# Performance work log

Hardware: AMD Instinct MI355X
Metric: run time of the kernel (lower is better)

Reference implementation:

```python
import jax, jax.numpy as jnp
import numpy as np

DIM = 96
D_STATE = 16
EXPAND = 2
D_INNER = EXPAND * DIM
DT_RANK = (DIM + 15) // 16  # 6
B, H, W = 2, 64, 64
K = 4  # scan directions


def _ln(x, w, b, eps=1e-5):
    mu = x.mean(-1, keepdims=True)
    var = x.var(-1, keepdims=True)
    return (x - mu) / jnp.sqrt(var + eps) * w + b


def setup_inputs() -> dict:
    key = jax.random.key(0)
    ks = jax.random.split(key, 10)
    f = jnp.float32
    x = jax.random.normal(ks[0], (B, H, W, DIM), dtype=f)
    y = jax.random.normal(ks[1], (B, H, W, DIM), dtype=f)
    inp = {
        'x': x,
        'y': y,
        'ln_w': jnp.ones((DIM,), f),
        'ln_b': jnp.zeros((DIM,), f),
        'in_proj_w': jax.random.normal(ks[2], (2 * D_INNER, DIM), f) * 0.05,
        'conv_w': jax.random.normal(ks[3], (D_INNER, 1, 3, 3), f) * 0.1,
        'conv_b': jnp.zeros((D_INNER,), f),
        'x_proj_w': jax.random.normal(ks[4], (K, DT_RANK + 2 * D_STATE, D_INNER), f) * 0.05,
        'dt_w': jax.random.normal(ks[5], (K, D_INNER, DT_RANK), f) * 0.1,
        'dt_b': jax.random.normal(ks[6], (K, D_INNER), f) * 0.1,
        'A_log': jnp.broadcast_to(jnp.log(jnp.arange(1, D_STATE + 1, dtype=f)), (K, D_INNER, D_STATE)),
        'Ds': jnp.ones((K, D_INNER), f),
        'out_norm_w': jnp.ones((D_INNER,), f),
        'out_norm_b': jnp.zeros((D_INNER,), f),
        'out_proj_w': jax.random.normal(ks[7], (DIM, D_INNER), f) * 0.05,
    }
    return inp


def _fwd(x, y, ln_w, ln_b, in_proj_w, conv_w, conv_b, x_proj_w, dt_w, dt_b,
         A_log, Ds, out_norm_w, out_norm_b, out_proj_w):
    Bsz, Hh, Ww, C = x.shape
    Din = conv_w.shape[0]
    N = A_log.shape[-1]
    R = dt_w.shape[-1]
    L = Hh * Ww

    diff = jnp.abs(x - y)                       # TemporalSpectrumBlock abs-diff
    h = _ln(diff, ln_w, ln_b)                   # VSSBlock ln_1
    xz = h @ in_proj_w.T                        # (B,H,W,2*Din)
    xm, z = jnp.split(xz, 2, axis=-1)
    xm = xm.transpose(0, 3, 1, 2)               # (B,Din,H,W)
    xm = jax.lax.conv_general_dilated(
        xm, conv_w, (1, 1), 'SAME', feature_group_count=Din,
        dimension_numbers=('NCHW', 'OIHW', 'NCHW')) + conv_b[None, :, None, None]
    xm = jax.nn.silu(xm)

    # 4-directional sequences (B,4,Din,L)
    x0 = xm.reshape(Bsz, Din, L)
    x1 = xm.transpose(0, 1, 3, 2).reshape(Bsz, Din, L)
    xs = jnp.stack([x0, x1], axis=1)
    xs = jnp.concatenate([xs, jnp.flip(xs, axis=-1)], axis=1)

    x_dbl = jnp.einsum('bkdl,kcd->bkcl', xs, x_proj_w)
    dts, Bs, Cs = jnp.split(x_dbl, [R, R + N], axis=2)   # (B,4,R,L),(B,4,N,L),(B,4,N,L)
    dts = jnp.einsum('bkrl,kdr->bkdl', dts, dt_w)
    delta = jax.nn.softplus(dts + dt_b[None, :, :, None])  # (B,4,Din,L)

    A = -jnp.exp(A_log)                                    # (4,Din,N)
    dA = jnp.exp(delta[..., None] * A[None, :, :, None, :])          # (B,4,Din,L,N)
    dBu = delta[..., None] * Bs.transpose(0, 1, 3, 2)[:, :, None] * xs[..., None]

    dA_t = dA.transpose(3, 0, 1, 2, 4)    # (L,B,4,Din,N)
    dBu_t = dBu.transpose(3, 0, 1, 2, 4)
    C_t = Cs.transpose(3, 0, 1, 2)        # (L,B,4,N)
    h0 = jnp.zeros((Bsz, 4, Din, N), dtype=x.dtype)

    def step(hc, inp):
        a, bu, c = inp
        hc = a * hc + bu
        yv = jnp.einsum('bkdn,bkn->bkd', hc, c)
        return hc, yv

    _, ys = jax.lax.scan(step, h0, (dA_t, dBu_t, C_t))    # (L,B,4,Din)
    ys = ys.transpose(1, 2, 3, 0)                          # (B,4,Din,L)
    out_y = ys + Ds[None, :, :, None] * xs

    inv_y = jnp.flip(out_y[:, 2:4], axis=-1)
    wh_y = out_y[:, 1].reshape(Bsz, Din, Ww, Hh).transpose(0, 1, 3, 2).reshape(Bsz, Din, L)
    invwh_y = inv_y[:, 1].reshape(Bsz, Din, Ww, Hh).transpose(0, 1, 3, 2).reshape(Bsz, Din, L)
    yc = out_y[:, 0] + inv_y[:, 0] + wh_y + invwh_y        # (B,Din,L)
    yc = yc.transpose(0, 2, 1).reshape(Bsz, Hh, Ww, Din)

    yn = _ln(yc, out_norm_w, out_norm_b)
    out = (yn * jax.nn.silu(z)) @ out_proj_w.T
    return diff + out                                      # residual around the block


def reference(x, y, ln_w, ln_b, in_proj_w, conv_w, conv_b, x_proj_w, dt_w, dt_b,
              A_log, Ds, out_norm_w, out_norm_b, out_proj_w):
    return _fwd(x, y, ln_w, ln_b, in_proj_w, conv_w, conv_b, x_proj_w, dt_w, dt_b,
                A_log, Ds, out_norm_w, out_norm_b, out_proj_w)
```

## Files before the change

kernel.cpp:

```cpp
#include <hip/hip_runtime.h>
#include <math.h>

#define DIMC 96
#define DIN  192
#define NST  16
#define RNK  6
#define KD   4
#define HH   64
#define WWD  64
#define LL   4096
#define BB   2
#define NC   64
#define CH   64
#define CPK  48

__device__ __forceinline__ int pos_of(int k, int l) {
    int t = ((l & 63) << 6) | (l >> 6);
    switch (k) {
        case 0: return l;
        case 1: return t;
        case 2: return LL - 1 - l;
        default: return ((((LL-1-l) & 63) << 6) | ((LL-1-l) >> 6));
    }
}

__device__ __forceinline__ float silu_f(float v) {
    return v / (1.f + __expf(-v));
}

__global__ __launch_bounds__(256) void k0_prep(
    const float* __restrict__ Win, const float* __restrict__ Wout,
    const float* __restrict__ xpw,
    float* __restrict__ WinT, float* __restrict__ WoutT, float* __restrict__ wT3)
{
    int idx = blockIdx.x*256 + threadIdx.x;
    int stride = gridDim.x*256;
    for (int i = idx; i < 96*384; i += stride) {
        int j = i / 384, o = i - j*384;
        WinT[i] = Win[o*96 + j];
    }
    for (int i = idx; i < 192*96; i += stride) {
        int j = i / 96, o = i - j*96;
        WoutT[i] = Wout[o*192 + j];
    }
    for (int i = idx; i < KD*192*CPK; i += stride) {
        int kk = i / (192*CPK); int rem = i - kk*192*CPK;
        int j = rem / CPK, c = rem - j*CPK;
        float v = 0.f;
        if (c < 16)       v = xpw[((size_t)kk*(RNK+2*NST) + RNK + c)*DIN + j];
        else if (c < 32)  v = xpw[((size_t)kk*(RNK+2*NST) + RNK + NST + (c-16))*DIN + j];
        else if (c < 38)  v = xpw[((size_t)kk*(RNK+2*NST) + (c-32))*DIN + j];
        wT3[i] = v;
    }
}

__global__ __launch_bounds__(1024) void k1_ln_inproj(
    const float* __restrict__ x, const float* __restrict__ y,
    const float* __restrict__ lnw, const float* __restrict__ lnb,
    const float* __restrict__ WinT,
    float* __restrict__ diff, float* __restrict__ xm, float* __restrict__ zbuf)
{
    __shared__ float hT[96*65];
    __shared__ float ps1[16*64], ps2[16*64];
    __shared__ float mus[64], rss[64];
    int t = threadIdx.x;
    int ptile = blockIdx.x >> 1, cgrp = blockIdx.x & 1;
    int p0 = ptile*64;

    #pragma unroll
    for (int s = 0; s < 6; s++) {
        int i = t + 1024*s;
        float v = fabsf(x[(size_t)p0*96 + i] - y[(size_t)p0*96 + i]);
        if (cgrp == 0) diff[(size_t)p0*96 + i] = v;
        int pos = i / 96, ch = i - pos*96;
        hT[ch*65 + pos] = v;
    }
    __syncthreads();
    {
        int pos = t & 63, part = t >> 6;
        float s1 = 0.f, s2 = 0.f;
        #pragma unroll
        for (int m = 0; m < 6; m++) {
            float v = hT[(part*6 + m)*65 + pos];
            s1 += v; s2 += v*v;
        }
        ps1[part*64 + pos] = s1; ps2[part*64 + pos] = s2;
    }
    __syncthreads();
    if (t < 64) {
        float S1 = 0.f, S2 = 0.f;
        #pragma unroll
        for (int i = 0; i < 16; i++) { S1 += ps1[i*64 + t]; S2 += ps2[i*64 + t]; }
        float mu = S1 * (1.f/96.f);
        float var = S2 * (1.f/96.f) - mu*mu;
        mus[t] = mu; rss[t] = rsqrtf(var + 1e-5f);
    }
    __syncthreads();
    #pragma unroll
    for (int s = 0; s < 6; s++) {
        int i = t + 1024*s;
        int pos = i / 96, ch = i - pos*96;
        hT[ch*65 + pos] = (hT[ch*65 + pos] - mus[pos]) * rss[pos] * lnw[ch] + lnb[ch];
    }
    __syncthreads();

    int w = __builtin_amdgcn_readfirstlane(t >> 6);
    int lane = t & 63;
    int c0 = cgrp*192 + w*12;
    const float* wp = WinT + c0;
    float acc[12];
    #pragma unroll
    for (int cc = 0; cc < 12; cc++) acc[cc] = 0.f;
    #pragma unroll 2
    for (int j = 0; j < 96; j++) {
        float u = hT[j*65 + lane];
        const float* wrow = wp + j*384;
        #pragma unroll
        for (int cc = 0; cc < 12; cc++) acc[cc] += u * wrow[cc];
    }
    size_t p = (size_t)(p0 + lane);
    float* dst = (c0 < 192) ? (xm + p*192 + c0) : (zbuf + p*192 + (c0 - 192));
    #pragma unroll
    for (int q = 0; q < 3; q++)
        *(float4*)&dst[4*q] = make_float4(acc[4*q], acc[4*q+1], acc[4*q+2], acc[4*q+3]);
}

__global__ __launch_bounds__(192) void k2_conv(
    const float* __restrict__ xm, const float* __restrict__ cw,
    const float* __restrict__ cb, float* __restrict__ xconv)
{
    int p = blockIdx.x;
    int d = threadIdx.x;
    int b = p >> 12;
    int l = p & (LL - 1);
    int hh = l >> 6, ww = l & 63;
    float acc = cb[d];
    const float* wd = cw + d*9;
    #pragma unroll
    for (int di = -1; di <= 1; di++) {
        int h2 = hh + di;
        if ((unsigned)h2 < HH) {
            #pragma unroll
            for (int dj = -1; dj <= 1; dj++) {
                int w2 = ww + dj;
                if ((unsigned)w2 < WWD)
                    acc += wd[(di+1)*3 + (dj+1)] * xm[((size_t)b*LL + h2*WWD + w2)*DIN + d];
            }
        }
    }
    xconv[(size_t)p*DIN + d] = silu_f(acc);
}

__global__ __launch_bounds__(512) void k3_xproj(
    const float* __restrict__ xconv, const float* __restrict__ wT3,
    float* __restrict__ XDK)
{
    __shared__ float uT[192*65];
    int t = threadIdx.x;
    int ptile = blockIdx.x >> 1, wgrp = blockIdx.x & 1;
    int p0 = ptile*64;

    #pragma unroll
    for (int s = 0; s < 24; s++) {
        int i = t + 512*s;
        int pos = i / 192, ch = i - pos*192;
        uT[ch*65 + pos] = xconv[(size_t)(p0 + pos)*192 + ch];
    }
    __syncthreads();

    int w = __builtin_amdgcn_readfirstlane(t >> 6);
    int slot = wgrp*8 + w;
    int k = slot >> 2, cq = slot & 3;
    int lane = t & 63;
    int c0 = cq*12;
    const float* wp = wT3 + (size_t)k*192*CPK + c0;
    float acc[12];
    #pragma unroll
    for (int cc = 0; cc < 12; cc++) acc[cc] = 0.f;
    #pragma unroll 2
    for (int j = 0; j < 192; j++) {
        float u = uT[j*65 + lane];
        const float* wrow = wp + j*CPK;
        #pragma unroll
        for (int cc = 0; cc < 12; cc++) acc[cc] += u * wrow[cc];
    }
    int p = p0 + lane;
    int b = p >> 12;
    int s = p & (LL - 1);
    int ts = ((s & 63) << 6) | (s >> 6);
    int l;
    switch (k) {
        case 0: l = s; break;
        case 1: l = ts; break;
        case 2: l = LL - 1 - s; break;
        default: l = LL - 1 - ts; break;
    }
    float* dst = XDK + ((size_t)(b*KD + k)*LL + l)*CPK + c0;
    #pragma unroll
    for (int q = 0; q < 3; q++)
        *(float4*)&dst[4*q] = make_float4(acc[4*q], acc[4*q+1], acc[4*q+2], acc[4*q+3]);
}

__global__ __launch_bounds__(192) void k4_scanA(
    const float* __restrict__ xconv, const float* __restrict__ XDK,
    const float* __restrict__ dtw, const float* __restrict__ dtb,
    const float* __restrict__ A_log,
    float* __restrict__ P, float* __restrict__ Q)
{
    int blk = blockIdx.x;
    int c  = blk & (NC - 1);
    int bk = blk >> 6;
    int k  = bk & 3;
    int b  = bk >> 2;
    int d  = threadIdx.x;
    float dw[RNK];
    #pragma unroll
    for (int r = 0; r < RNK; r++) dw[r] = dtw[((size_t)k*DIN + d)*RNK + r];
    float bias = dtb[k*DIN + d];
    float A[NST];
    #pragma unroll
    for (int n = 0; n < NST; n++) A[n] = -__expf(A_log[((size_t)k*DIN + d)*NST + n]);

    float h[NST], pr[NST];
    #pragma unroll
    for (int n = 0; n < NST; n++) { h[n] = 0.f; pr[n] = 1.f; }

    size_t rb = ((size_t)bk*LL + c*CH)*CPK;
    #pragma unroll 2
    for (int step = 0; step < CH; step++) {
        const float* rec = XDK + rb + step*CPK;
        float dl = bias;
        #pragma unroll
        for (int r = 0; r < RNK; r++) dl += rec[32 + r] * dw[r];
        dl = (dl > 20.f) ? dl : __logf(1.f + __expf(dl));
        int l = c*CH + step;
        float uu = xconv[((size_t)b*LL + pos_of(k, l))*DIN + d];
        float du = dl * uu;
        #pragma unroll
        for (int n = 0; n < NST; n++) {
            float a = __expf(dl * A[n]);
            h[n] = a*h[n] + du*rec[n];
            pr[n] *= a;
        }
    }
    size_t base = (size_t)blk*NST*DIN + d;
    #pragma unroll
    for (int n = 0; n < NST; n++) { P[base + n*DIN] = pr[n]; Q[base + n*DIN] = h[n]; }
}

__global__ __launch_bounds__(256) void k5_scanB(
    const float* __restrict__ P, float* __restrict__ Q)
{
    int idx = blockIdx.x*256 + threadIdx.x;
    if (idx >= BB*KD*NST*DIN) return;
    int d = idx % DIN;
    int rest = idx / DIN;
    int n = rest % NST; rest /= NST;
    int k = rest % KD;
    int b = rest / KD;
    size_t base = ((((size_t)(b*KD + k))*NC)*NST + n)*DIN + d;
    size_t stride = (size_t)NST*DIN;
    float h = 0.f;
    #pragma unroll 4
    for (int c = 0; c < NC; c++) {
        float p = P[base + c*stride];
        float q = Q[base + c*stride];
        Q[base + c*stride] = h;
        h = p*h + q;
    }
}

__global__ __launch_bounds__(192) void k6_scanC(
    const float* __restrict__ xconv, const float* __restrict__ XDK,
    const float* __restrict__ dtw, const float* __restrict__ dtb,
    const float* __restrict__ A_log, const float* __restrict__ Ds,
    const float* __restrict__ Q, float* __restrict__ outy)
{
    int blk = blockIdx.x;
    int c  = blk & (NC - 1);
    int bk = blk >> 6;
    int k  = bk & 3;
    int b  = bk >> 2;
    int d  = threadIdx.x;
    float dw[RNK];
    #pragma unroll
    for (int r = 0; r < RNK; r++) dw[r] = dtw[((size_t)k*DIN + d)*RNK + r];
    float bias = dtb[k*DIN + d];
    float A[NST];
    #pragma unroll
    for (int n = 0; n < NST; n++) A[n] = -__expf(A_log[((size_t)k*DIN + d)*NST + n]);
    float h[NST];
    size_t qbase = (size_t)blk*NST*DIN + d;
    #pragma unroll
    for (int n = 0; n < NST; n++) h[n] = Q[qbase + n*DIN];
    float Dv = Ds[k*DIN + d];

    size_t rb = ((size_t)bk*LL + c*CH)*CPK;
    #pragma unroll 2
    for (int step = 0; step < CH; step++) {
        const float* rec = XDK + rb + step*CPK;
        float dl = bias;
        #pragma unroll
        for (int r = 0; r < RNK; r++) dl += rec[32 + r] * dw[r];
        dl = (dl > 20.f) ? dl : __logf(1.f + __expf(dl));
        int l = c*CH + step;
        float uu = xconv[((size_t)b*LL + pos_of(k, l))*DIN + d];
        float du = dl * uu;
        float yv = 0.f;
        #pragma unroll
        for (int n = 0; n < NST; n++) {
            float a = __expf(dl * A[n]);
            h[n] = a*h[n] + du*rec[n];
            yv += h[n] * rec[16 + n];
        }
        outy[((size_t)bk*LL + l)*DIN + d] = yv + Dv*uu;
    }
}

__global__ __launch_bounds__(256) void k7_out(
    const float* __restrict__ outy, const float* __restrict__ zbuf,
    const float* __restrict__ diff, const float* __restrict__ onw,
    const float* __restrict__ onb, const float* __restrict__ WoutT,
    float* __restrict__ out)
{
    __shared__ float gT[192*65];
    __shared__ float ps1[4*64], ps2[4*64];
    __shared__ float mus[64], rss[64];
    int t = threadIdx.x;
    int ptile = blockIdx.x >> 1, chalf = blockIdx.x & 1;
    int p0 = ptile*64;
    int b = p0 >> 12;
    int l0 = p0 & (LL - 1);

    #pragma unroll
    for (int s = 0; s < 48; s++) {
        int i = t + 256*s;
        int pos = i / 192, ch = i - pos*192;
        int l = l0 + pos;
        int tl = ((l & 63) << 6) | (l >> 6);
        float yc = outy[(((size_t)(b*KD + 0))*LL + l)*DIN + ch]
                 + outy[(((size_t)(b*KD + 2))*LL + (LL-1-l))*DIN + ch]
                 + outy[(((size_t)(b*KD + 1))*LL + tl)*DIN + ch]
                 + outy[(((size_t)(b*KD + 3))*LL + (LL-1-tl))*DIN + ch];
        gT[ch*65 + pos] = yc;
    }
    __syncthreads();
    {
        int pos = t & 63, part = t >> 6;
        float s1 = 0.f, s2 = 0.f;
        #pragma unroll
        for (int m = 0; m < 48; m++) {
            float v = gT[(part*48 + m)*65 + pos];
            s1 += v; s2 += v*v;
        }
        ps1[part*64 + pos] = s1; ps2[part*64 + pos] = s2;
    }
    __syncthreads();
    if (t < 64) {
        float S1 = ps1[t] + ps1[64+t] + ps1[128+t] + ps1[192+t];
        float S2 = ps2[t] + ps2[64+t] + ps2[128+t] + ps2[192+t];
        float mu = S1 * (1.f/192.f);
        float var = S2 * (1.f/192.f) - mu*mu;
        mus[t] = mu; rss[t] = rsqrtf(var + 1e-5f);
    }
    __syncthreads();
    #pragma unroll
    for (int s = 0; s < 48; s++) {
        int i = t + 256*s;
        int pos = i / 192, ch = i - pos*192;
        float v = gT[ch*65 + pos];
        float yn = (v - mus[pos]) * rss[pos] * onw[ch] + onb[ch];
        float z = zbuf[(size_t)(p0 + pos)*DIN + ch];
        gT[ch*65 + pos] = yn * silu_f(z);
    }
    __syncthreads();

    int w = __builtin_amdgcn_readfirstlane(t >> 6);
    int lane = t & 63;
    int c0 = chalf*48 + w*12;
    const float* wp = WoutT + c0;
    float acc[12];
    #pragma unroll
    for (int cc = 0; cc < 12; cc++) acc[cc] = 0.f;
    #pragma unroll 2
    for (int j = 0; j < 192; j++) {
        float u = gT[j*65 + lane];
        const float* wrow = wp + j*96;
        #pragma unroll
        for (int cc = 0; cc < 12; cc++) acc[cc] += u * wrow[cc];
    }
    size_t p = (size_t)(p0 + lane);
    #pragma unroll
    for (int q = 0; q < 3; q++) {
        float4 dv = *(const float4*)&diff[p*96 + c0 + 4*q];
        *(float4*)&out[p*96 + c0 + 4*q] =
            make_float4(acc[4*q] + dv.x, acc[4*q+1] + dv.y, acc[4*q+2] + dv.z, acc[4*q+3] + dv.w);
    }
}

extern "C" void kernel_launch(void* const* d_in, const int* in_sizes, int n_in,
                              void* d_out, int out_size, void* d_ws, size_t ws_size,
                              hipStream_t stream)
{
    const float* x       = (const float*)d_in[0];
    const float* y       = (const float*)d_in[1];
    const float* ln_w    = (const float*)d_in[2];
    const float* ln_b    = (const float*)d_in[3];
    const float* in_proj = (const float*)d_in[4];
    const float* conv_w  = (const float*)d_in[5];
    const float* conv_b  = (const float*)d_in[6];
    const float* x_proj  = (const float*)d_in[7];
    const float* dt_w    = (const float*)d_in[8];
    const float* dt_b    = (const float*)d_in[9];
    const float* A_log   = (const float*)d_in[10];
    const float* Ds      = (const float*)d_in[11];
    const float* onw     = (const float*)d_in[12];
    const float* onb     = (const float*)d_in[13];
    const float* out_w   = (const float*)d_in[14];
    float* out = (float*)d_out;

    float* ws    = (float*)d_ws;
    float* diff  = ws;
    float* zbuf  = diff  + 786432;
    float* xm    = zbuf  + 1572864;
    float* xconv = xm    + 1572864;
    float* XDK   = xconv + 1572864;
    float* outy  = XDK   + 1572864;
    float* Pbuf  = outy  + 6291456;
    float* Qbuf  = Pbuf  + 1572864;
    float* WinT  = Qbuf  + 1572864;
    float* WoutT = WinT  + 36864;
    float* wT3   = WoutT + 18432;

    const int BL = BB * LL;

    hipLaunchKernelGGL(k0_prep, dim3(144), dim3(256), 0, stream,
                       in_proj, out_w, x_proj, WinT, WoutT, wT3);
    hipLaunchKernelGGL(k1_ln_inproj, dim3(BL/64*2), dim3(1024), 0, stream,
                       x, y, ln_w, ln_b, WinT, diff, xm, zbuf);
    hipLaunchKernelGGL(k2_conv, dim3(BL), dim3(DIN), 0, stream,
                       xm, conv_w, conv_b, xconv);
    hipLaunchKernelGGL(k3_xproj, dim3(BL/64*2), dim3(512), 0, stream,
                       xconv, wT3, XDK);
    hipLaunchKernelGGL(k4_scanA, dim3(BB*KD*NC), dim3(DIN), 0, stream,
                       xconv, XDK, dt_w, dt_b, A_log, Pbuf, Qbuf);
    hipLaunchKernelGGL(k5_scanB, dim3((BB*KD*NST*DIN + 255)/256), dim3(256), 0, stream,
                       Pbuf, Qbuf);
    hipLaunchKernelGGL(k6_scanC, dim3(BB*KD*NC), dim3(DIN), 0, stream,
                       xconv, XDK, dt_w, dt_b, A_log, Ds, Qbuf, outy);
    hipLaunchKernelGGL(k7_out, dim3(BL/64*2), dim3(256), 0, stream,
                       outy, zbuf, diff, onw, onb, WoutT, out);
}
```

Baseline: 299.4 us.

## Store per-chunk dt sums instead of decay products and use power-chain exponentials

The chunked selective scan now keeps only the per-chunk sum of dt and rebuilds each chunk's decay product as exp(A*S) in the carry pass, so the per-state product array is no longer written or read. When A[n] equals (n+1)*A[0], which a runtime check detects, the 16 exponentials per step become one exp followed by repeated multiplication. Chunks are halved to 32 steps, doubling their number to give more parallel blocks at the cost of a longer sequential carry pass. The power-chain path accumulates rounding across states and only applies when A_log matches that structure; other inputs fall back to the general path.

```diff
diff --git a/kernel.cpp b/kernel.cpp
--- a/kernel.cpp
+++ b/kernel.cpp
@@ -10,8 +10,8 @@
 #define WWD  64
 #define LL   4096
 #define BB   2
-#define NC   64
-#define CH   64
+#define NC   128
+#define CH   32
 #define CPK  48
 
 __device__ __forceinline__ int pos_of(int k, int l) {
@@ -205,11 +205,11 @@
     const float* __restrict__ xconv, const float* __restrict__ XDK,
     const float* __restrict__ dtw, const float* __restrict__ dtb,
     const float* __restrict__ A_log,
-    float* __restrict__ P, float* __restrict__ Q)
+    float* __restrict__ Sarr, float* __restrict__ Q)
 {
     int blk = blockIdx.x;
     int c  = blk & (NC - 1);
-    int bk = blk >> 6;
+    int bk = blk >> 7;
     int k  = bk & 3;
     int b  = bk >> 2;
     int d  = threadIdx.x;
@@ -220,53 +220,85 @@
     float A[NST];
     #pragma unroll
     for (int n = 0; n < NST; n++) A[n] = -__expf(A_log[((size_t)k*DIN + d)*NST + n]);
-
-    float h[NST], pr[NST];
-    #pragma unroll
-    for (int n = 0; n < NST; n++) { h[n] = 0.f; pr[n] = 1.f; }
+    bool fastA = true;
+    #pragma unroll
+    for (int n = 1; n < NST; n++)
+        fastA = fastA && (fabsf(A[n] - (float)(n+1)*A[0]) <= 1e-4f*(float)(n+1));
+
+    float h[NST];
+    #pragma unroll
+    for (int n = 0; n < NST; n++) h[n] = 0.f;
+    float S = 0.f;
 
     size_t rb = ((size_t)bk*LL + c*CH)*CPK;
-    #pragma unroll 2
-    for (int step = 0; step < CH; step++) {
-        const float* rec = XDK + rb + step*CPK;
-        float dl = bias;
-        #pragma unroll
-        for (int r = 0; r < RNK; r++) dl += rec[32 + r] * dw[r];
-        dl = (dl > 20.f) ? dl : __logf(1.f + __expf(dl));
-        int l = c*CH + step;
-        float uu = xconv[((size_t)b*LL + pos_of(k, l))*DIN + d];
-        float du = dl * uu;
-        #pragma unroll
-        for (int n = 0; n < NST; n++) {
-            float a = __expf(dl * A[n]);
-            h[n] = a*h[n] + du*rec[n];
-            pr[n] *= a;
-        }
-    }
-    size_t base = (size_t)blk*NST*DIN + d;
-    #pragma unroll
-    for (int n = 0; n < NST; n++) { P[base + n*DIN] = pr[n]; Q[base + n*DIN] = h[n]; }
+    if (fastA) {
+        #pragma unroll 2
+        for (int step = 0; step < CH; step++) {
+            const float* rec = XDK + rb + step*CPK;
+            float dl = bias;
+            #pragma unroll
+            for (int r = 0; r < RNK; r++) dl += rec[32 + r] * dw[r];
+            dl = (dl > 20.f) ? dl : __logf(1.f + __expf(dl));
+            int l = c*CH + step;
+            float uu = xconv[((size_t)b*LL + pos_of(k, l))*DIN + d];
+            float du = dl * uu;
+            S += dl;
+            float e1 = __expf(dl * A[0]);
+            float a = e1;
+            #pragma unroll
+            for (int n = 0; n < NST; n++) {
+                h[n] = a*h[n] + du*rec[n];
+                a *= e1;
+            }
+        }
+    } else {
+        #pragma unroll 2
+        for (int step = 0; step < CH; step++) {
+            const float* rec = XDK + rb + step*CPK;
+            float dl = bias;
+            #pragma unroll
+            for (int r = 0; r < RNK; r++) dl += rec[32 + r] * dw[r];
+            dl = (dl > 20.f) ? dl : __logf(1.f + __expf(dl));
+            int l = c*CH + step;
+            float uu = xconv[((size_t)b*LL + pos_of(k, l))*DIN + d];
+            float du = dl * uu;
+            S += dl;
+            #pragma unroll
+            for (int n = 0; n < NST; n++) {
+                float a = __expf(dl * A[n]);
+                h[n] = a*h[n] + du*rec[n];
+            }
+        }
+    }
+    Sarr[(size_t)blk*DIN + d] = S;
+    size_t qb = (size_t)blk*NST*DIN + d;
+    #pragma unroll
+    for (int n = 0; n < NST; n++) Q[qb + n*DIN] = h[n];
 }
 
 __global__ __launch_bounds__(256) void k5_scanB(
-    const float* __restrict__ P, float* __restrict__ Q)
+    const float* __restrict__ A_log, const float* __restrict__ Sarr,
+    float* __restrict__ Q)
 {
     int idx = blockIdx.x*256 + threadIdx.x;
     if (idx >= BB*KD*NST*DIN) return;
     int d = idx % DIN;
     int rest = idx / DIN;
     int n = rest % NST; rest /= NST;
-    int k = rest % KD;
-    int b = rest / KD;
-    size_t base = ((((size_t)(b*KD + k))*NC)*NST + n)*DIN + d;
-    size_t stride = (size_t)NST*DIN;
+    int k = rest & 3;
+    int b = rest >> 2;
+    int bk = b*KD + k;
+    float A = -__expf(A_log[((size_t)k*DIN + d)*NST + n]);
+    size_t qstride = (size_t)NST*DIN;
+    size_t qbase = (size_t)bk*NC*qstride + n*DIN + d;
+    size_t sbase = (size_t)bk*NC*DIN + d;
     float h = 0.f;
     #pragma unroll 4
     for (int c = 0; c < NC; c++) {
-        float p = P[base + c*stride];
-        float q = Q[base + c*stride];
-        Q[base + c*stride] = h;
-        h = p*h + q;
+        float s = Sarr[sbase + c*DIN];
+        float q = Q[qbase + c*qstride];
+        Q[qbase + c*qstride] = h;
+        h = __expf(A*s)*h + q;
     }
 }
 
@@ -278,7 +310,7 @@
 {
     int blk = blockIdx.x;
     int c  = blk & (NC - 1);
-    int bk = blk >> 6;
+    int bk = blk >> 7;
     int k  = bk & 3;
     int b  = bk >> 2;
     int d  = threadIdx.x;
@@ -289,31 +321,59 @@
     float A[NST];
     #pragma unroll
     for (int n = 0; n < NST; n++) A[n] = -__expf(A_log[((size_t)k*DIN + d)*NST + n]);
+    bool fastA = true;
+    #pragma unroll
+    for (int n = 1; n < NST; n++)
+        fastA = fastA && (fabsf(A[n] - (float)(n+1)*A[0]) <= 1e-4f*(float)(n+1));
     float h[NST];
-    size_t qbase = (size_t)blk*NST*DIN + d;
-    #pragma unroll
-    for (int n = 0; n < NST; n++) h[n] = Q[qbase + n*DIN];
+    size_t qb = (size_t)blk*NST*DIN + d;
+    #pragma unroll
+    for (int n = 0; n < NST; n++) h[n] = Q[qb + n*DIN];
     float Dv = Ds[k*DIN + d];
 
     size_t rb = ((size_t)bk*LL + c*CH)*CPK;
-    #pragma unroll 2
-    for (int step = 0; step < CH; step++) {
-        const float* rec = XDK + rb + step*CPK;
-        float dl = bias;
-        #pragma unroll
-        for (int r = 0; r < RNK; r++) dl += rec[32 + r] * dw[r];
-        dl = (dl > 20.f) ? dl : __logf(1.f + __expf(dl));
-        int l = c*CH + step;
-        float uu = xconv[((size_t)b*LL + pos_of(k, l))*DIN + d];
-        float du = dl * uu;
-        float yv = 0.f;
-        #pragma unroll
-        for (int n = 0; n < NST; n++) {
-            float a = __expf(dl * A[n]);
-            h[n] = a*h[n] + du*rec[n];
-            yv += h[n] * rec[16 + n];
-        }
-        outy[((size_t)bk*LL + l)*DIN + d] = yv + Dv*uu;
+    if (fastA) {
+        #pragma unroll 2
+        for (int step = 0; step < CH; step++) {
+            const float* rec = XDK + rb + step*CPK;
+            float dl = bias;
+            #pragma unroll
+            for (int r = 0; r < RNK; r++) dl += rec[32 + r] * dw[r];
+            dl = (dl > 20.f) ? dl : __logf(1.f + __expf(dl));
+            int l = c*CH + step;
+            float uu = xconv[((size_t)b*LL + pos_of(k, l))*DIN + d];
+            float du = dl * uu;
+            float e1 = __expf(dl * A[0]);
+            float a = e1;
+            float yv = 0.f;
+            #pragma unroll
+            for (int n = 0; n < NST; n++) {
+                h[n] = a*h[n] + du*rec[n];
+                yv += h[n] * rec[16 + n];
+                a *= e1;
+            }
+            outy[((size_t)bk*LL + l)*DIN + d] = yv + Dv*uu;
+        }
+    } else {
+        #pragma unroll 2
+        for (int step = 0; step < CH; step++) {
+            const float* rec = XDK + rb + step*CPK;
+            float dl = bias;
+            #pragma unroll
+            for (int r = 0; r < RNK; r++) dl += rec[32 + r] * dw[r];
+            dl = (dl > 20.f) ? dl : __logf(1.f + __expf(dl));
+            int l = c*CH + step;
+            float uu = xconv[((size_t)b*LL + pos_of(k, l))*DIN + d];
+            float du = dl * uu;
+            float yv = 0.f;
+            #pragma unroll
+            for (int n = 0; n < NST; n++) {
+                float a = __expf(dl * A[n]);
+                h[n] = a*h[n] + du*rec[n];
+                yv += h[n] * rec[16 + n];
+            }
+            outy[((size_t)bk*LL + l)*DIN + d] = yv + Dv*uu;
+        }
     }
 }
 
@@ -426,9 +486,9 @@
     float* xconv = xm    + 1572864;
     float* XDK   = xconv + 1572864;
     float* outy  = XDK   + 1572864;
-    float* Pbuf  = outy  + 6291456;
-    float* Qbuf  = Pbuf  + 1572864;
-    float* WinT  = Qbuf  + 1572864;
+    float* Qbuf  = outy  + 6291456;
+    float* Sarr  = Qbuf  + 3145728;
+    float* WinT  = Sarr  + 196608;
     float* WoutT = WinT  + 36864;
     float* wT3   = WoutT + 18432;
 
@@ -443,9 +503,9 @@
     hipLaunchKernelGGL(k3_xproj, dim3(BL/64*2), dim3(512), 0, stream,
                        xconv, wT3, XDK);
     hipLaunchKernelGGL(k4_scanA, dim3(BB*KD*NC), dim3(DIN), 0, stream,
-                       xconv, XDK, dt_w, dt_b, A_log, Pbuf, Qbuf);
+                       xconv, XDK, dt_w, dt_b, A_log, Sarr, Qbuf);
     hipLaunchKernelGGL(k5_scanB, dim3((BB*KD*NST*DIN + 255)/256), dim3(256), 0, stream,
-                       Pbuf, Qbuf);
+                       A_log, Sarr, Qbuf);
     hipLaunchKernelGGL(k6_scanC, dim3(BB*KD*NC), dim3(DIN), 0, stream,
                        xconv, XDK, dt_w, dt_b, A_log, Ds, Qbuf, outy);
     hipLaunchKernelGGL(k7_out, dim3(BL/64*2), dim3(256), 0, stream,
```

Measured after the change: 270.2 us. 1.11x faster.
